# Kernel tuning notes

Hardware: AMD Instinct MI355X
Metric: run time of the kernel (lower is better)

Reference implementation:

```python
import jax, jax.numpy as jnp
import numpy as np

EPS = 0.01
H, W = 300, 400
WORLD_SCALE = 400.0


def setup_inputs() -> dict:
    key = jax.random.key(0)
    ks = jax.random.split(key, 8)
    N, B, D, HID = 200000, 2, 256, 256
    fx = fy = 300.0
    cx, cy = W / 2.0, H / 2.0
    z = jax.random.uniform(ks[0], (N,), minval=2.0, maxval=10.0)
    u = jax.random.uniform(ks[1], (N,), minval=0.0, maxval=float(W))
    v = jax.random.uniform(ks[2], (N,), minval=0.0, maxval=float(H))
    vert_pos = jnp.stack([(u - cx) / fx * z, (v - cy) / fy * z, z], axis=0)  # [3,N]
    target_pose = jnp.tile(jnp.eye(4, dtype=jnp.float32)[None], (B, 1, 1))
    K = jnp.array([[fx, 0.0, cx], [0.0, fy, cy], [0.0, 0.0, 1.0]], dtype=jnp.float32)
    target_intrinsics = jnp.tile(K[None], (B, 1, 1))
    vert_feat = 0.1 * jax.random.normal(ks[3], (N, D), dtype=jnp.float32)
    vert_opy = jnp.ones((N,), dtype=jnp.float32)
    W1 = 0.05 * jax.random.normal(ks[4], (D + 3, HID), dtype=jnp.float32)
    b1 = jnp.zeros((HID,), dtype=jnp.float32)
    W2 = 0.05 * jax.random.normal(ks[5], (HID, 3), dtype=jnp.float32)
    b2 = jnp.zeros((3,), dtype=jnp.float32)
    bkg_col = jnp.zeros((3,), dtype=jnp.float32)
    ref_images = jax.random.normal(ks[6], (B, 3, H, W), dtype=jnp.float32)
    return {"vert_pos": vert_pos, "ref_images": ref_images, "target_pose": target_pose,
            "target_intrinsics": target_intrinsics, "vert_feat": vert_feat, "vert_opy": vert_opy,
            "W1": W1, "b1": b1, "W2": W2, "b2": b2, "bkg_col": bkg_col}


def reference(vert_pos, ref_images, target_pose, target_intrinsics,
              vert_feat, vert_opy, W1, b1, W2, b2, bkg_col):
    B = target_pose.shape[0]
    N = vert_pos.shape[1]
    # homogeneous world points, transform to target camera frame
    xyzw = jnp.concatenate([vert_pos, jnp.ones((1, N), vert_pos.dtype)], axis=0)  # [4,N]
    xyz_t = jnp.einsum('bij,jn->bin', target_pose, xyzw)[:, :3]                   # [B,3,N]
    xy_proj = jnp.einsum('bij,bjn->bin', target_intrinsics, xyz_t)                # [B,3,N]
    z = xy_proj[:, 2:3]
    eps_mask = jax.lax.stop_gradient(jnp.abs(z) < EPS)                            # [B,1,N]
    zs = jnp.where(eps_mask, EPS, z)
    uv = xy_proj[:, 0:2] / zs
    sampler = jnp.where(eps_mask, -1e6, jnp.concatenate([uv, zs], axis=1))        # [B,3,N]
    # view direction in world frame per point
    vnorm = xyz_t / jnp.linalg.norm(xyz_t, axis=1, keepdims=True)
    vh = jnp.concatenate([vnorm, jnp.zeros_like(vnorm[:, 0:1])], axis=1)          # [B,4,N]
    pose_inv = jnp.linalg.inv(target_pose)
    vdir = jnp.einsum('bij,bjn->bin', pose_inv, vh)[:, :3]                        # [B,3,N]
    vdir = vdir.transpose(0, 2, 1).reshape(B * N, 3)
    # per-point neural shading (MLP shader on concat(feat, view_dir))
    feat = jnp.broadcast_to(vert_feat[None], (B, N, vert_feat.shape[1])).reshape(B * N, -1)
    x = jnp.concatenate([feat, vdir], axis=-1)
    h = jax.nn.relu(x @ W1 + b1)
    rgb = jax.nn.sigmoid(h @ W2 + b2).reshape(B, N, 3)                            # [B,N,3]
    opacity = jnp.clip(jax.nn.sigmoid(vert_opy), 0.0, 1.0)                        # [N]
    # differentiable splat: scatter shaded colors weighted by opacity to pixels
    u_pix, v_pix, zz = sampler[:, 0], sampler[:, 1], sampler[:, 2]                # [B,N]
    ix = jnp.round(u_pix).astype(jnp.int32)
    iy = jnp.round(v_pix).astype(jnp.int32)
    valid = (ix >= 0) & (ix < W) & (iy >= 0) & (iy < H) & (zz >= 1.0)
    idx = jnp.where(valid, iy * W + ix, H * W)                                    # dump bin H*W
    wts = opacity[None, :] * valid.astype(rgb.dtype)                              # [B,N]
    seg = lambda vals, ids: jax.ops.segment_sum(vals, ids, num_segments=H * W + 1)
    num = jax.vmap(seg)(wts[..., None] * rgb, idx)[:, :H * W]                     # [B,HW,3]
    den = jax.vmap(seg)(wts, idx)[:, :H * W]                                      # [B,HW]
    fg = num / (den[..., None] + 1e-8)
    alpha = 1.0 - jnp.exp(-den)
    img = fg * alpha[..., None] + bkg_col * (1.0 - alpha[..., None])
    return img.reshape(B, H, W, 3).transpose(0, 3, 1, 2)                          # [B,3,H,W]
```

## Files before the change

kernel.cpp:

```cpp
#include <hip/hip_runtime.h>
#include <cstdint>
#include <cstddef>

#define HH 300
#define WW 400
#define HWPIX (HH*WW)

typedef __attribute__((ext_vector_type(8))) short short8_t;
typedef __attribute__((ext_vector_type(4))) float f32x4;

static __device__ __forceinline__ unsigned short f2bf(float f){
  union { float f; unsigned u; } v; v.f = f;
  unsigned r = (v.u + 0x7fffu + ((v.u >> 16) & 1u)) >> 16;
  return (unsigned short)r;
}
static __device__ __forceinline__ float bf2f(unsigned short us){
  union { unsigned u; float f; } v; v.u = ((unsigned)us) << 16;
  return v.f;
}
static __device__ __forceinline__ float dot4_x(float a0,float x0,float a1,float x1,
                                               float a2,float x2,float a3,float x3){
  #pragma clang fp contract(off)
  float s = a0*x0;
  s = s + a1*x1;
  s = s + a2*x2;
  s = s + a3*x3;
  return s;
}
static __device__ __forceinline__ float dot3_x(float a0,float x0,float a1,float x1,
                                               float a2,float x2){
  #pragma clang fp contract(off)
  float s = a0*x0;
  s = s + a1*x1;
  s = s + a2*x2;
  return s;
}

static __device__ __forceinline__ void gload_lds16(const void* g, void* l){
  __builtin_amdgcn_global_load_lds(
      (const __attribute__((address_space(1))) unsigned int*)g,
      (__attribute__((address_space(3))) unsigned int*)l, 16, 0, 0);
}

static __device__ __forceinline__ void atomAddF32(float* p, float v){
  unsafeAtomicAdd(p, v);
}

__global__ void prep_kernel(const float* __restrict__ W1, const float* __restrict__ W2,
                            const float* __restrict__ pose,
                            float* __restrict__ poseinv, unsigned short* __restrict__ W1aT,
                            float* __restrict__ ntab, int B){
  int tid = threadIdx.x;
  int bid = blockIdx.x;
  if (bid < 256){
    int n = bid, k = tid;
    int kt = k >> 6;
    int c8 = (k >> 3) & 7;
    int i  = k & 7;
    W1aT[kt*16384 + n*64 + ((c8 ^ (n & 7))<<3) + i] = f2bf(W1[k*256 + n]);
  } else {
    int n = tid;
    ntab[n*8+0] = W1[256*256 + n];
    ntab[n*8+1] = W1[257*256 + n];
    ntab[n*8+2] = W1[258*256 + n];
    ntab[n*8+3] = W2[n*3+0];
    ntab[n*8+4] = W2[n*3+1];
    ntab[n*8+5] = W2[n*3+2];
    ntab[n*8+6] = 0.f; ntab[n*8+7] = 0.f;
    if (tid < B){
      float M[4][8];
      const float* A = pose + tid*16;
      for (int i=0;i<4;i++) for (int j=0;j<4;j++){ M[i][j]=A[i*4+j]; M[i][4+j] = (i==j)?1.f:0.f; }
      for (int c=0;c<4;c++){
        int p=c;
        for (int r=c+1;r<4;r++) if (fabsf(M[r][c])>fabsf(M[p][c])) p=r;
        if (p!=c) for (int j=0;j<8;j++){ float t=M[c][j]; M[c][j]=M[p][j]; M[p][j]=t; }
        float inv = 1.f/M[c][c];
        for (int j=0;j<8;j++) M[c][j]*=inv;
        for (int r=0;r<4;r++) if (r!=c){ float f=M[r][c]; for(int j=0;j<8;j++) M[r][j]-=f*M[c][j]; }
      }
      float* O = poseinv + tid*16;
      for (int i=0;i<4;i++) for (int j=0;j<4;j++) O[i*4+j]=M[i][4+j];
    }
  }
}

__global__ __launch_bounds__(256) void mlp_scatter_kernel(
    const float* __restrict__ feat, const unsigned short* __restrict__ W1aT,
    const float* __restrict__ b1, const float* __restrict__ b2,
    const float* __restrict__ ntab,
    const float* __restrict__ vp, const float* __restrict__ opy,
    const float* __restrict__ pose, const float* __restrict__ intr,
    const float* __restrict__ poseinv,
    float* __restrict__ num, float* __restrict__ den, int N, int B)
{
  __shared__ __align__(16) char smem[40960];
  unsigned short* sA = (unsigned short*)smem;
  unsigned short* sB = (unsigned short*)(smem + 8192);
  unsigned short* sH = (unsigned short*)smem;
  float* part        = (float*)(smem + 32768);

  const int tid  = threadIdx.x;
  const int lane = tid & 63;
  const int wv   = __builtin_amdgcn_readfirstlane(tid >> 6);
  const int lr   = lane & 15;
  const int qd   = lane >> 4;
  const int m0   = blockIdx.x * 64;

  f32x4 acc[4][4];
  for (int i=0;i<4;i++) for (int j=0;j<4;j++) acc[i][j] = (f32x4){0.f,0.f,0.f,0.f};

  ushort4 uA[4];
  {
    #pragma unroll
    for (int i=0;i<4;i++){
      int q   = i*256 + tid;
      int row = q >> 4;
      int c4  = q & 15;
      long rg = m0 + row; if (rg >= N) rg = N-1;
      float4 f = *(const float4*)(feat + rg*256 + c4*4);
      ushort4 u; u.x = f2bf(f.x); u.y = f2bf(f.y); u.z = f2bf(f.z); u.w = f2bf(f.w);
      uA[i] = u;
    }
  }

  for (int kt=0; kt<4; kt++){
    #pragma unroll
    for (int i=0;i<4;i++){
      int q   = i*256 + tid;
      int row = q >> 4;
      int c4  = q & 15;
      int q8 = c4 >> 1, half = c4 & 1;
      int phys = q8 ^ (row & 7);
      *(ushort4*)(sA + row*64 + phys*8 + half*4) = uA[i];
    }
    {
      const unsigned int* gim = (const unsigned int*)(W1aT + kt*16384);
      unsigned int* lim = (unsigned int*)sB;
      #pragma unroll
      for (int i=0;i<8;i++)
        gload_lds16(gim + i*1024 + tid*4, lim + i*1024 + tid*4);
    }
    __syncthreads();

    if (kt < 3){
      #pragma unroll
      for (int i=0;i<4;i++){
        int q   = i*256 + tid;
        int row = q >> 4;
        int c4  = q & 15;
        long rg = m0 + row; if (rg >= N) rg = N-1;
        float4 f = *(const float4*)(feat + rg*256 + (kt+1)*64 + c4*4);
        ushort4 u; u.x = f2bf(f.x); u.y = f2bf(f.y); u.z = f2bf(f.z); u.w = f2bf(f.w);
        uA[i] = u;
      }
    }

    #pragma unroll
    for (int ks=0; ks<2; ks++){
      short8_t av[4], bv[4];
      int qlog = ks*4 + qd;
      #pragma unroll
      for (int mt=0; mt<4; mt++){
        int row  = mt*16 + lr;
        int phys = qlog ^ (row & 7);
        av[mt] = *(const short8_t*)(sA + row*64 + phys*8);
      }
      #pragma unroll
      for (int nt=0; nt<4; nt++){
        int n    = wv*64 + nt*16 + lr;
        int phys = qlog ^ (n & 7);
        bv[nt] = *(const short8_t*)(sB + n*64 + phys*8);
      }
      #pragma unroll
      for (int mt=0; mt<4; mt++)
        #pragma unroll
        for (int nt=0; nt<4; nt++)
          acc[mt][nt] = __builtin_amdgcn_mfma_f32_16x16x32_bf16(av[mt], bv[nt], acc[mt][nt], 0,0,0);
    }
    __syncthreads();
  }

  #pragma unroll
  for (int nt=0; nt<4; nt++){
    int n = wv*64 + nt*16 + lr;
    float bias = b1[n];
    int c = n >> 3, e = n & 7;
    #pragma unroll
    for (int mt=0; mt<4; mt++)
      #pragma unroll
      for (int rr=0; rr<4; rr++){
        int m = mt*16 + qd*4 + rr;
        sH[m*256 + ((c ^ (m & 7))<<3) + e] = f2bf(acc[mt][nt][rr] + bias);
      }
  }
  __syncthreads();

  const int r = lane;
  long vg = m0 + r;
  bool rowok = vg < N; if (!rowok) vg = N-1;
  float px = vp[vg], py = vp[(size_t)N+vg], pz = vp[2*(size_t)N+vg];
  const float* tb = ntab + (size_t)wv*64*8;
  const int rsw = r & 7;
  const unsigned short* hrow = sH + r*256;
  float opac = 1.f/(1.f+expf(-opy[vg]));

  short8_t hv[8];
  #pragma unroll
  for (int j8=0;j8<8;j8++){
    int c = wv*8 + j8;
    hv[j8] = *(const short8_t*)(hrow + ((c ^ rsw)<<3));
  }

  for (int b0=0; b0<B; b0+=2){
    int nb = (B - b0 < 2) ? (B - b0) : 2;
    float s_up=-1e6f, s_vp=-1e6f, s_zz=-1e6f;
    for (int bi=0; bi<nb; bi++){
      int b = b0 + bi;
      const float* P  = pose + b*16;
      const float* Kc = intr + b*9;
      const float* Pi = poseinv + b*16;
      float xt = dot4_x(P[0],px, P[1],py, P[2], pz, P[3], 1.f);
      float yt = dot4_x(P[4],px, P[5],py, P[6], pz, P[7], 1.f);
      float zt = dot4_x(P[8],px, P[9],py, P[10],pz, P[11],1.f);
      float uu = dot3_x(Kc[0],xt, Kc[1],yt, Kc[2],zt);
      float vv = dot3_x(Kc[3],xt, Kc[4],yt, Kc[5],zt);
      float zp = dot3_x(Kc[6],xt, Kc[7],yt, Kc[8],zt);
      bool em = fabsf(zp) < 0.01f;
      float zsafe = em ? 0.01f : zp;
      float up   = em ? -1e6f : uu/zsafe;
      float vpix = em ? -1e6f : vv/zsafe;
      float zz   = em ? -1e6f : zsafe;
      if (bi == wv){ s_up = up; s_vp = vpix; s_zz = zz; }
      float inrm = 1.f/sqrtf(xt*xt + yt*yt + zt*zt);
      float nx=xt*inrm, ny=yt*inrm, nz=zt*inrm;
      float vdx = Pi[0]*nx + Pi[1]*ny + Pi[2]*nz;
      float vdy = Pi[4]*nx + Pi[5]*ny + Pi[6]*nz;
      float vdz = Pi[8]*nx + Pi[9]*ny + Pi[10]*nz;

      float a0=0.f, a1=0.f, a2=0.f;
      #pragma unroll
      for (int j8=0;j8<8;j8++){
        const float* t = tb + j8*64;
        #pragma unroll
        for (int e=0;e<8;e++){
          float h = bf2f((unsigned short)hv[j8][e]) + vdx*t[e*8+0] + vdy*t[e*8+1] + vdz*t[e*8+2];
          h = fmaxf(h, 0.f);
          a0 += h*t[e*8+3]; a1 += h*t[e*8+4]; a2 += h*t[e*8+5];
        }
      }
      part[bi*768 + (wv*64 + r)*3 + 0] = a0;
      part[bi*768 + (wv*64 + r)*3 + 1] = a1;
      part[bi*768 + (wv*64 + r)*3 + 2] = a2;
    }
    __syncthreads();
    if (wv < nb){
      int b = b0 + wv;
      const float* pp = part + wv*768;
      float s0 = pp[r*3+0] + pp[(64+r)*3+0] + pp[(128+r)*3+0] + pp[(192+r)*3+0];
      float s1 = pp[r*3+1] + pp[(64+r)*3+1] + pp[(128+r)*3+1] + pp[(192+r)*3+1];
      float s2 = pp[r*3+2] + pp[(64+r)*3+2] + pp[(128+r)*3+2] + pp[(192+r)*3+2];
      float r0 = 1.f/(1.f+expf(-(s0 + b2[0])));
      float r1 = 1.f/(1.f+expf(-(s1 + b2[1])));
      float r2 = 1.f/(1.f+expf(-(s2 + b2[2])));
      int ix = (int)rintf(s_up);
      int iy = (int)rintf(s_vp);
      bool valid = rowok && ix>=0 && ix<WW && iy>=0 && iy<HH && s_zz>=1.0f;
      if (valid){
        int idx = iy*WW + ix;
        atomAddF32(den + (size_t)b*HWPIX + idx, opac);
        atomAddF32(num + ((size_t)b*3+0)*HWPIX + idx, opac*r0);
        atomAddF32(num + ((size_t)b*3+1)*HWPIX + idx, opac*r1);
        atomAddF32(num + ((size_t)b*3+2)*HWPIX + idx, opac*r2);
      }
    }
    __syncthreads();
  }
}

__global__ void compose_kernel(float* __restrict__ out, const float* __restrict__ den,
                               const float* __restrict__ bkg, int B){
  int i = blockIdx.x*256 + threadIdx.x;
  int total = B*HWPIX;
  if (i >= total) return;
  int b = i / HWPIX;
  int pix = i - b*HWPIX;
  float d = den[i];
  float alpha = 1.f - expf(-d);
  float om = 1.f - alpha;
  float dd = d + 1e-8f;
  float* ob = out + (size_t)b*3*HWPIX;
  float f0 = ob[0*HWPIX + pix] / dd;
  float f1 = ob[1*HWPIX + pix] / dd;
  float f2 = ob[2*HWPIX + pix] / dd;
  ob[0*HWPIX + pix] = f0*alpha + bkg[0]*om;
  ob[1*HWPIX + pix] = f1*alpha + bkg[1]*om;
  ob[2*HWPIX + pix] = f2*alpha + bkg[2]*om;
}

extern "C" void kernel_launch(void* const* d_in, const int* in_sizes, int n_in,
                              void* d_out, int out_size, void* d_ws, size_t ws_size,
                              hipStream_t stream){
  const float* vp   = (const float*)d_in[0];
  const float* pose = (const float*)d_in[2];
  const float* intr = (const float*)d_in[3];
  const float* feat = (const float*)d_in[4];
  const float* opy  = (const float*)d_in[5];
  const float* W1   = (const float*)d_in[6];
  const float* b1   = (const float*)d_in[7];
  const float* W2   = (const float*)d_in[8];
  const float* b2   = (const float*)d_in[9];
  const float* bkg  = (const float*)d_in[10];
  float* out = (float*)d_out;
  int N = in_sizes[0]/3;
  int B = in_sizes[2]/16;

  char* ws = (char*)d_ws;
  float* poseinv        = (float*)ws;
  unsigned short* W1aT  = (unsigned short*)(ws + 256);
  float* ntab           = (float*)(ws + 256 + 131072);
  float* den            = (float*)(ws + 256 + 131072 + 8192);

  hipMemsetAsync(out, 0, (size_t)out_size*sizeof(float), stream);
  hipMemsetAsync(den, 0, (size_t)B*HWPIX*sizeof(float), stream);
  prep_kernel<<<257, 256, 0, stream>>>(W1, W2, pose, poseinv, W1aT, ntab, B);
  int gridM = (N + 63)/64;
  mlp_scatter_kernel<<<gridM, 256, 0, stream>>>(feat, W1aT, b1, b2, ntab, vp, opy,
                                                pose, intr, poseinv, out, den, N, B);
  compose_kernel<<<(B*HWPIX + 255)/256, 256, 0, stream>>>(out, den, bkg, B);
}
```

Measured before the change: 436.8 us.

## Read W1 fragments from global memory directly and stage full A tile once

The per-k-tile LDS staging of the bf16 W1 tile is removed. Each wave now reads its B fragments for the MFMA straight from a plain transposed W1 layout in global memory (L2/cache resident). All four feature k-slices are loaded into registers up front and written to LDS once, which cuts the K loop down to a single barrier. The epilogue splits the atomics across all four waves instead of two, the output zeroing is folded into prep_kernel in place of a memset, and the trailing barrier is skipped on the final batch iteration. The trade-off is higher register pressure from the 16 float4 loads and uncoalesced per-lane global B loads.

Result: slower. 492.9 us (+12.9%).

```diff
diff --git a/kernel.cpp b/kernel.cpp
--- a/kernel.cpp
+++ b/kernel.cpp
@@ -36,12 +36,6 @@
   return s;
 }
 
-static __device__ __forceinline__ void gload_lds16(const void* g, void* l){
-  __builtin_amdgcn_global_load_lds(
-      (const __attribute__((address_space(1))) unsigned int*)g,
-      (__attribute__((address_space(3))) unsigned int*)l, 16, 0, 0);
-}
-
 static __device__ __forceinline__ void atomAddF32(float* p, float v){
   unsafeAtomicAdd(p, v);
 }
@@ -49,15 +43,19 @@
 __global__ void prep_kernel(const float* __restrict__ W1, const float* __restrict__ W2,
                             const float* __restrict__ pose,
                             float* __restrict__ poseinv, unsigned short* __restrict__ W1aT,
-                            float* __restrict__ ntab, int B){
+                            float* __restrict__ ntab,
+                            float* __restrict__ zbuf, int zcount4, int B){
   int tid = threadIdx.x;
   int bid = blockIdx.x;
+  {
+    float4 z = {0.f,0.f,0.f,0.f};
+    int stride = gridDim.x * blockDim.x;
+    for (int i = bid*blockDim.x + tid; i < zcount4; i += stride)
+      ((float4*)zbuf)[i] = z;
+  }
   if (bid < 256){
     int n = bid, k = tid;
-    int kt = k >> 6;
-    int c8 = (k >> 3) & 7;
-    int i  = k & 7;
-    W1aT[kt*16384 + n*64 + ((c8 ^ (n & 7))<<3) + i] = f2bf(W1[k*256 + n]);
+    W1aT[n*256 + k] = f2bf(W1[k*256 + n]);
   } else {
     int n = tid;
     ntab[n*8+0] = W1[256*256 + n];
@@ -94,9 +92,8 @@
     const float* __restrict__ poseinv,
     float* __restrict__ num, float* __restrict__ den, int N, int B)
 {
-  __shared__ __align__(16) char smem[40960];
+  __shared__ __align__(16) char smem[38912];
   unsigned short* sA = (unsigned short*)smem;
-  unsigned short* sB = (unsigned short*)(smem + 8192);
   unsigned short* sH = (unsigned short*)smem;
   float* part        = (float*)(smem + 32768);
 
@@ -107,70 +104,55 @@
   const int qd   = lane >> 4;
   const int m0   = blockIdx.x * 64;
 
-  f32x4 acc[4][4];
-  for (int i=0;i<4;i++) for (int j=0;j<4;j++) acc[i][j] = (f32x4){0.f,0.f,0.f,0.f};
-
-  ushort4 uA[4];
   {
-    #pragma unroll
-    for (int i=0;i<4;i++){
-      int q   = i*256 + tid;
-      int row = q >> 4;
-      int c4  = q & 15;
-      long rg = m0 + row; if (rg >= N) rg = N-1;
-      float4 f = *(const float4*)(feat + rg*256 + c4*4);
-      ushort4 u; u.x = f2bf(f.x); u.y = f2bf(f.y); u.z = f2bf(f.z); u.w = f2bf(f.w);
-      uA[i] = u;
-    }
-  }
-
-  for (int kt=0; kt<4; kt++){
-    #pragma unroll
-    for (int i=0;i<4;i++){
-      int q   = i*256 + tid;
-      int row = q >> 4;
-      int c4  = q & 15;
-      int q8 = c4 >> 1, half = c4 & 1;
-      int phys = q8 ^ (row & 7);
-      *(ushort4*)(sA + row*64 + phys*8 + half*4) = uA[i];
-    }
-    {
-      const unsigned int* gim = (const unsigned int*)(W1aT + kt*16384);
-      unsigned int* lim = (unsigned int*)sB;
-      #pragma unroll
-      for (int i=0;i<8;i++)
-        gload_lds16(gim + i*1024 + tid*4, lim + i*1024 + tid*4);
-    }
-    __syncthreads();
-
-    if (kt < 3){
+    float4 fr[16];
+    #pragma unroll
+    for (int s=0;s<4;s++)
       #pragma unroll
       for (int i=0;i<4;i++){
         int q   = i*256 + tid;
         int row = q >> 4;
         int c4  = q & 15;
         long rg = m0 + row; if (rg >= N) rg = N-1;
-        float4 f = *(const float4*)(feat + rg*256 + (kt+1)*64 + c4*4);
+        fr[s*4+i] = *(const float4*)(feat + rg*256 + s*64 + c4*4);
+      }
+    #pragma unroll
+    for (int s=0;s<4;s++)
+      #pragma unroll
+      for (int i=0;i<4;i++){
+        int q   = i*256 + tid;
+        int row = q >> 4;
+        int c4  = q & 15;
+        float4 f = fr[s*4+i];
         ushort4 u; u.x = f2bf(f.x); u.y = f2bf(f.y); u.z = f2bf(f.z); u.w = f2bf(f.w);
-        uA[i] = u;
-      }
-    }
-
+        int q8 = c4 >> 1, half = c4 & 1;
+        int phys = q8 ^ (row & 7);
+        *(ushort4*)(sA + s*4096 + row*64 + phys*8 + half*4) = u;
+      }
+  }
+  __syncthreads();
+
+  f32x4 acc[4][4];
+  #pragma unroll
+  for (int i=0;i<4;i++)
+    #pragma unroll
+    for (int j=0;j<4;j++) acc[i][j] = (f32x4){0.f,0.f,0.f,0.f};
+
+  const unsigned short* Wb = W1aT + (size_t)(wv*64)*256;
+  #pragma unroll
+  for (int kt=0; kt<4; kt++){
     #pragma unroll
     for (int ks=0; ks<2; ks++){
+      int qlog = ks*4 + qd;
       short8_t av[4], bv[4];
-      int qlog = ks*4 + qd;
+      #pragma unroll
+      for (int nt=0; nt<4; nt++)
+        bv[nt] = *(const short8_t*)(Wb + (nt*16 + lr)*256 + kt*64 + qlog*8);
       #pragma unroll
       for (int mt=0; mt<4; mt++){
         int row  = mt*16 + lr;
         int phys = qlog ^ (row & 7);
-        av[mt] = *(const short8_t*)(sA + row*64 + phys*8);
-      }
-      #pragma unroll
-      for (int nt=0; nt<4; nt++){
-        int n    = wv*64 + nt*16 + lr;
-        int phys = qlog ^ (n & 7);
-        bv[nt] = *(const short8_t*)(sB + n*64 + phys*8);
+        av[mt] = *(const short8_t*)(sA + kt*4096 + row*64 + phys*8);
       }
       #pragma unroll
       for (int mt=0; mt<4; mt++)
@@ -178,8 +160,8 @@
         for (int nt=0; nt<4; nt++)
           acc[mt][nt] = __builtin_amdgcn_mfma_f32_16x16x32_bf16(av[mt], bv[nt], acc[mt][nt], 0,0,0);
     }
-    __syncthreads();
-  }
+  }
+  __syncthreads();
 
   #pragma unroll
   for (int nt=0; nt<4; nt++){
@@ -231,7 +213,7 @@
       float up   = em ? -1e6f : uu/zsafe;
       float vpix = em ? -1e6f : vv/zsafe;
       float zz   = em ? -1e6f : zsafe;
-      if (bi == wv){ s_up = up; s_vp = vpix; s_zz = zz; }
+      if (bi == (wv & 1)){ s_up = up; s_vp = vpix; s_zz = zz; }
       float inrm = 1.f/sqrtf(xt*xt + yt*yt + zt*zt);
       float nx=xt*inrm, ny=yt*inrm, nz=zt*inrm;
       float vdx = Pi[0]*nx + Pi[1]*ny + Pi[2]*nz;
@@ -254,27 +236,30 @@
       part[bi*768 + (wv*64 + r)*3 + 2] = a2;
     }
     __syncthreads();
-    if (wv < nb){
-      int b = b0 + wv;
-      const float* pp = part + wv*768;
-      float s0 = pp[r*3+0] + pp[(64+r)*3+0] + pp[(128+r)*3+0] + pp[(192+r)*3+0];
-      float s1 = pp[r*3+1] + pp[(64+r)*3+1] + pp[(128+r)*3+1] + pp[(192+r)*3+1];
-      float s2 = pp[r*3+2] + pp[(64+r)*3+2] + pp[(128+r)*3+2] + pp[(192+r)*3+2];
-      float r0 = 1.f/(1.f+expf(-(s0 + b2[0])));
-      float r1 = 1.f/(1.f+expf(-(s1 + b2[1])));
-      float r2 = 1.f/(1.f+expf(-(s2 + b2[2])));
+    if ((wv & 1) < nb){
+      int b = b0 + (wv & 1);
+      const float* pp = part + (wv & 1)*768;
       int ix = (int)rintf(s_up);
       int iy = (int)rintf(s_vp);
       bool valid = rowok && ix>=0 && ix<WW && iy>=0 && iy<HH && s_zz>=1.0f;
       if (valid){
         int idx = iy*WW + ix;
-        atomAddF32(den + (size_t)b*HWPIX + idx, opac);
-        atomAddF32(num + ((size_t)b*3+0)*HWPIX + idx, opac*r0);
-        atomAddF32(num + ((size_t)b*3+1)*HWPIX + idx, opac*r1);
-        atomAddF32(num + ((size_t)b*3+2)*HWPIX + idx, opac*r2);
+        if (wv < 2){
+          float s0 = pp[r*3+0] + pp[(64+r)*3+0] + pp[(128+r)*3+0] + pp[(192+r)*3+0];
+          float r0 = 1.f/(1.f+expf(-(s0 + b2[0])));
+          atomAddF32(den + (size_t)b*HWPIX + idx, opac);
+          atomAddF32(num + ((size_t)b*3+0)*HWPIX + idx, opac*r0);
+        } else {
+          float s1 = pp[r*3+1] + pp[(64+r)*3+1] + pp[(128+r)*3+1] + pp[(192+r)*3+1];
+          float s2 = pp[r*3+2] + pp[(64+r)*3+2] + pp[(128+r)*3+2] + pp[(192+r)*3+2];
+          float r1 = 1.f/(1.f+expf(-(s1 + b2[1])));
+          float r2 = 1.f/(1.f+expf(-(s2 + b2[2])));
+          atomAddF32(num + ((size_t)b*3+1)*HWPIX + idx, opac*r1);
+          atomAddF32(num + ((size_t)b*3+2)*HWPIX + idx, opac*r2);
+        }
       }
     }
-    __syncthreads();
+    if (b0 + 2 < B) __syncthreads();
   }
 }
 
@@ -321,9 +306,9 @@
   float* ntab           = (float*)(ws + 256 + 131072);
   float* den            = (float*)(ws + 256 + 131072 + 8192);
 
-  hipMemsetAsync(out, 0, (size_t)out_size*sizeof(float), stream);
+  prep_kernel<<<257, 256, 0, stream>>>(W1, W2, pose, poseinv, W1aT, ntab,
+                                       out, (B*3*HWPIX)/4, B);
   hipMemsetAsync(den, 0, (size_t)B*HWPIX*sizeof(float), stream);
-  prep_kernel<<<257, 256, 0, stream>>>(W1, W2, pose, poseinv, W1aT, ntab, B);
   int gridM = (N + 63)/64;
   mlp_scatter_kernel<<<gridM, 256, 0, stream>>>(feat, W1aT, b1, b2, ntab, vp, opy,
                                                 pose, intr, poseinv, out, den, N, B);
```

## Fuse both batch views into one MLP-head loop and split scatter atomics across waves

Applied to the files above, without the earlier changes.

The per-vertex view-dependent head now handles both batch views in a single pass over the hidden units, so each ntab weight entry is loaded once and reused for two views instead of reloaded per view. The scatter work is split so all four waves issue atomics (two channels each) instead of only two waves doing four atomics. Accumulation moves to a workspace buffer with one memset, and compose reads from it rather than rewriting out in place. The prep kernel's transposed-write indexing is swapped for more coalesced global reads of W1. The cost is higher register pressure from six accumulators, and wasted work when B is odd.

Measured after the change: 414.2 us. 5.2% less time.

```diff
diff --git a/kernel.cpp b/kernel.cpp
--- a/kernel.cpp
+++ b/kernel.cpp
@@ -53,7 +53,7 @@
   int tid = threadIdx.x;
   int bid = blockIdx.x;
   if (bid < 256){
-    int n = bid, k = tid;
+    int k = bid, n = tid;
     int kt = k >> 6;
     int c8 = (k >> 3) & 7;
     int i  = k & 7;
@@ -214,71 +214,87 @@
 
   for (int b0=0; b0<B; b0+=2){
     int nb = (B - b0 < 2) ? (B - b0) : 2;
-    float s_up=-1e6f, s_vp=-1e6f, s_zz=-1e6f;
-    for (int bi=0; bi<nb; bi++){
-      int b = b0 + bi;
-      const float* P  = pose + b*16;
-      const float* Kc = intr + b*9;
-      const float* Pi = poseinv + b*16;
-      float xt = dot4_x(P[0],px, P[1],py, P[2], pz, P[3], 1.f);
-      float yt = dot4_x(P[4],px, P[5],py, P[6], pz, P[7], 1.f);
-      float zt = dot4_x(P[8],px, P[9],py, P[10],pz, P[11],1.f);
-      float uu = dot3_x(Kc[0],xt, Kc[1],yt, Kc[2],zt);
-      float vv = dot3_x(Kc[3],xt, Kc[4],yt, Kc[5],zt);
-      float zp = dot3_x(Kc[6],xt, Kc[7],yt, Kc[8],zt);
-      bool em = fabsf(zp) < 0.01f;
-      float zsafe = em ? 0.01f : zp;
-      float up   = em ? -1e6f : uu/zsafe;
-      float vpix = em ? -1e6f : vv/zsafe;
-      float zz   = em ? -1e6f : zsafe;
-      if (bi == wv){ s_up = up; s_vp = vpix; s_zz = zz; }
-      float inrm = 1.f/sqrtf(xt*xt + yt*yt + zt*zt);
-      float nx=xt*inrm, ny=yt*inrm, nz=zt*inrm;
-      float vdx = Pi[0]*nx + Pi[1]*ny + Pi[2]*nz;
-      float vdy = Pi[4]*nx + Pi[5]*ny + Pi[6]*nz;
-      float vdz = Pi[8]*nx + Pi[9]*ny + Pi[10]*nz;
-
-      float a0=0.f, a1=0.f, a2=0.f;
-      #pragma unroll
-      for (int j8=0;j8<8;j8++){
-        const float* t = tb + j8*64;
-        #pragma unroll
-        for (int e=0;e<8;e++){
-          float h = bf2f((unsigned short)hv[j8][e]) + vdx*t[e*8+0] + vdy*t[e*8+1] + vdz*t[e*8+2];
-          h = fmaxf(h, 0.f);
-          a0 += h*t[e*8+3]; a1 += h*t[e*8+4]; a2 += h*t[e*8+5];
-        }
-      }
-      part[bi*768 + (wv*64 + r)*3 + 0] = a0;
-      part[bi*768 + (wv*64 + r)*3 + 1] = a1;
-      part[bi*768 + (wv*64 + r)*3 + 2] = a2;
+    float vdx0=0.f, vdy0=0.f, vdz0=0.f, sup0=-1e6f, svp0=-1e6f, szz0=-1e6f;
+    float vdx1=0.f, vdy1=0.f, vdz1=0.f, sup1=-1e6f, svp1=-1e6f, szz1=-1e6f;
+    #pragma unroll
+    for (int bi=0; bi<2; bi++){
+      if (bi < nb){
+        int b = b0 + bi;
+        const float* P  = pose + b*16;
+        const float* Kc = intr + b*9;
+        const float* Pi = poseinv + b*16;
+        float xt = dot4_x(P[0],px, P[1],py, P[2], pz, P[3], 1.f);
+        float yt = dot4_x(P[4],px, P[5],py, P[6], pz, P[7], 1.f);
+        float zt = dot4_x(P[8],px, P[9],py, P[10],pz, P[11],1.f);
+        float uu = dot3_x(Kc[0],xt, Kc[1],yt, Kc[2],zt);
+        float vv = dot3_x(Kc[3],xt, Kc[4],yt, Kc[5],zt);
+        float zp = dot3_x(Kc[6],xt, Kc[7],yt, Kc[8],zt);
+        bool em = fabsf(zp) < 0.01f;
+        float zsafe = em ? 0.01f : zp;
+        float up   = em ? -1e6f : uu/zsafe;
+        float vpix = em ? -1e6f : vv/zsafe;
+        float zz   = em ? -1e6f : zsafe;
+        float inrm = 1.f/sqrtf(xt*xt + yt*yt + zt*zt);
+        float nx=xt*inrm, ny=yt*inrm, nz=zt*inrm;
+        float vx = Pi[0]*nx + Pi[1]*ny + Pi[2]*nz;
+        float vy = Pi[4]*nx + Pi[5]*ny + Pi[6]*nz;
+        float vz = Pi[8]*nx + Pi[9]*ny + Pi[10]*nz;
+        if (bi == 0){ vdx0=vx; vdy0=vy; vdz0=vz; sup0=up; svp0=vpix; szz0=zz; }
+        else        { vdx1=vx; vdy1=vy; vdz1=vz; sup1=up; svp1=vpix; szz1=zz; }
+      }
+    }
+    float a00=0.f,a01=0.f,a02=0.f, a10=0.f,a11=0.f,a12=0.f;
+    #pragma unroll
+    for (int j8=0;j8<8;j8++){
+      #pragma unroll
+      for (int e=0;e<8;e++){
+        const float* t = tb + (j8*8+e)*8;
+        float t0=t[0], t1=t[1], t2=t[2], t3=t[3], t4=t[4], t5=t[5];
+        float hb = bf2f((unsigned short)hv[j8][e]);
+        float h0 = fmaxf(hb + vdx0*t0 + vdy0*t1 + vdz0*t2, 0.f);
+        float h1 = fmaxf(hb + vdx1*t0 + vdy1*t1 + vdz1*t2, 0.f);
+        a00 += h0*t3; a01 += h0*t4; a02 += h0*t5;
+        a10 += h1*t3; a11 += h1*t4; a12 += h1*t5;
+      }
+    }
+    {
+      int base = (wv*64 + r)*3;
+      part[base+0] = a00; part[base+1] = a01; part[base+2] = a02;
+      part[768+base+0] = a10; part[768+base+1] = a11; part[768+base+2] = a12;
     }
     __syncthreads();
-    if (wv < nb){
-      int b = b0 + wv;
-      const float* pp = part + wv*768;
-      float s0 = pp[r*3+0] + pp[(64+r)*3+0] + pp[(128+r)*3+0] + pp[(192+r)*3+0];
-      float s1 = pp[r*3+1] + pp[(64+r)*3+1] + pp[(128+r)*3+1] + pp[(192+r)*3+1];
-      float s2 = pp[r*3+2] + pp[(64+r)*3+2] + pp[(128+r)*3+2] + pp[(192+r)*3+2];
-      float r0 = 1.f/(1.f+expf(-(s0 + b2[0])));
-      float r1 = 1.f/(1.f+expf(-(s1 + b2[1])));
-      float r2 = 1.f/(1.f+expf(-(s2 + b2[2])));
-      int ix = (int)rintf(s_up);
-      int iy = (int)rintf(s_vp);
-      bool valid = rowok && ix>=0 && ix<WW && iy>=0 && iy<HH && s_zz>=1.0f;
+    if ((wv & 1) < nb){
+      int b = b0 + (wv & 1);
+      const float* pp = part + (wv & 1)*768;
+      float S_up = (wv & 1) ? sup1 : sup0;
+      float S_vp = (wv & 1) ? svp1 : svp0;
+      float S_zz = (wv & 1) ? szz1 : szz0;
+      int ix = (int)rintf(S_up);
+      int iy = (int)rintf(S_vp);
+      bool valid = rowok && ix>=0 && ix<WW && iy>=0 && iy<HH && S_zz>=1.0f;
       if (valid){
         int idx = iy*WW + ix;
-        atomAddF32(den + (size_t)b*HWPIX + idx, opac);
-        atomAddF32(num + ((size_t)b*3+0)*HWPIX + idx, opac*r0);
-        atomAddF32(num + ((size_t)b*3+1)*HWPIX + idx, opac*r1);
-        atomAddF32(num + ((size_t)b*3+2)*HWPIX + idx, opac*r2);
-      }
-    }
-    __syncthreads();
-  }
-}
-
-__global__ void compose_kernel(float* __restrict__ out, const float* __restrict__ den,
+        if (wv < 2){
+          float s0 = pp[r*3+0] + pp[(64+r)*3+0] + pp[(128+r)*3+0] + pp[(192+r)*3+0];
+          float r0 = 1.f/(1.f+expf(-(s0 + b2[0])));
+          atomAddF32(den + (size_t)b*HWPIX + idx, opac);
+          atomAddF32(num + ((size_t)b*3+0)*HWPIX + idx, opac*r0);
+        } else {
+          float s1 = pp[r*3+1] + pp[(64+r)*3+1] + pp[(128+r)*3+1] + pp[(192+r)*3+1];
+          float s2 = pp[r*3+2] + pp[(64+r)*3+2] + pp[(128+r)*3+2] + pp[(192+r)*3+2];
+          float r1 = 1.f/(1.f+expf(-(s1 + b2[1])));
+          float r2 = 1.f/(1.f+expf(-(s2 + b2[2])));
+          atomAddF32(num + ((size_t)b*3+1)*HWPIX + idx, opac*r1);
+          atomAddF32(num + ((size_t)b*3+2)*HWPIX + idx, opac*r2);
+        }
+      }
+    }
+    if (b0 + 2 < B) __syncthreads();
+  }
+}
+
+__global__ void compose_kernel(float* __restrict__ out, const float* __restrict__ num,
+                               const float* __restrict__ den,
                                const float* __restrict__ bkg, int B){
   int i = blockIdx.x*256 + threadIdx.x;
   int total = B*HWPIX;
@@ -289,13 +305,11 @@
   float alpha = 1.f - expf(-d);
   float om = 1.f - alpha;
   float dd = d + 1e-8f;
+  const float* nb_ = num + (size_t)b*3*HWPIX;
   float* ob = out + (size_t)b*3*HWPIX;
-  float f0 = ob[0*HWPIX + pix] / dd;
-  float f1 = ob[1*HWPIX + pix] / dd;
-  float f2 = ob[2*HWPIX + pix] / dd;
-  ob[0*HWPIX + pix] = f0*alpha + bkg[0]*om;
-  ob[1*HWPIX + pix] = f1*alpha + bkg[1]*om;
-  ob[2*HWPIX + pix] = f2*alpha + bkg[2]*om;
+  ob[0*HWPIX + pix] = (nb_[0*HWPIX + pix]/dd)*alpha + bkg[0]*om;
+  ob[1*HWPIX + pix] = (nb_[1*HWPIX + pix]/dd)*alpha + bkg[1]*om;
+  ob[2*HWPIX + pix] = (nb_[2*HWPIX + pix]/dd)*alpha + bkg[2]*om;
 }
 
 extern "C" void kernel_launch(void* const* d_in, const int* in_sizes, int n_in,
@@ -319,13 +333,13 @@
   float* poseinv        = (float*)ws;
   unsigned short* W1aT  = (unsigned short*)(ws + 256);
   float* ntab           = (float*)(ws + 256 + 131072);
-  float* den            = (float*)(ws + 256 + 131072 + 8192);
-
-  hipMemsetAsync(out, 0, (size_t)out_size*sizeof(float), stream);
-  hipMemsetAsync(den, 0, (size_t)B*HWPIX*sizeof(float), stream);
+  float* num            = (float*)(ws + 256 + 131072 + 8192);
+  float* den            = num + (size_t)B*3*HWPIX;
+
+  hipMemsetAsync(num, 0, (size_t)B*4*HWPIX*sizeof(float), stream);
   prep_kernel<<<257, 256, 0, stream>>>(W1, W2, pose, poseinv, W1aT, ntab, B);
   int gridM = (N + 63)/64;
   mlp_scatter_kernel<<<gridM, 256, 0, stream>>>(feat, W1aT, b1, b2, ntab, vp, opy,
-                                                pose, intr, poseinv, out, den, N, B);
-  compose_kernel<<<(B*HWPIX + 255)/256, 256, 0, stream>>>(out, den, bkg, B);
-}
+                                                pose, intr, poseinv, num, den, N, B);
+  compose_kernel<<<(B*HWPIX + 255)/256, 256, 0, stream>>>(out, num, den, bkg, B);
+}
```
